# Kernel optimization log

Measured on AMD Instinct MI355X. Metric: run time of the kernel, lower is better.

Reference implementation:

```python
import jax, jax.numpy as jnp
import numpy as np

MARGIN_POS = 1.0
MARGIN_NEG = 0.2
LAMBDA_D = 250.0

B, D, H, W = 2, 128, 64, 64


def setup_inputs() -> dict:
    key = jax.random.key(0)
    k0, k1, k2 = jax.random.split(key, 3)
    descriptors_0 = jax.random.normal(k0, (B, D, H, W), dtype=jnp.float32)
    descriptors_1 = jax.random.normal(k1, (B, D, H, W), dtype=jnp.float32)
    similarity_mask = jax.random.randint(k2, (B, H, W, H, W), 0, 2).astype(jnp.bool_)
    return {
        "descriptors_0": descriptors_0,
        "descriptors_1": descriptors_1,
        "similarity_mask": similarity_mask,
    }


def reference(descriptors_0, descriptors_1, similarity_mask):
    # [B,D,H,W] x [B,D,H,W] -> [B,H,W,H,W] dense pairwise descriptor dot products
    dotprod = jnp.einsum('bdij,bdkl->bijkl', descriptors_0, descriptors_1)
    zero = jnp.zeros((), dtype=dotprod.dtype)
    pos_loss = jnp.maximum(zero, MARGIN_POS - dotprod) * LAMBDA_D
    neg_loss = jnp.maximum(zero, dotprod - MARGIN_NEG)
    return jnp.where(similarity_mask, pos_loss, neg_loss).mean()
```

## Files before the change

kernel.cpp:

```cpp
#include <hip/hip_runtime.h>
#include <hip/hip_bf16.h>
#include <stdint.h>

#define BN 2
#define DN 128
#define MN 4096
#define TOTAL_INV (1.0f / 33554432.0f)

typedef __attribute__((ext_vector_type(8))) short short8;
typedef __attribute__((ext_vector_type(4))) float f32x4;

__device__ static inline unsigned short f2bf(float x) {
  unsigned int u = __float_as_uint(x);
  u += 0x7fffu + ((u >> 16) & 1u);
  return (unsigned short)(u >> 16);
}

__device__ static inline void async16(const void* g, void* l) {
  __builtin_amdgcn_global_load_lds(
      (const __attribute__((address_space(1))) void*)g,
      (__attribute__((address_space(3))) void*)l, 16, 0, 0);
}

__global__ __launch_bounds__(256) void transpose_cvt(
    const float* __restrict__ s0, const float* __restrict__ s1,
    unsigned short* __restrict__ o0, unsigned short* __restrict__ o1) {
  __shared__ float tile[64][65];
  const int tx = threadIdx.x & 63;
  const int ty = threadIdx.x >> 6;
  const int m0 = blockIdx.x * 64;
  const int d0 = blockIdx.y * 64;
  const int b  = blockIdx.z & 1;
  const float* src = (blockIdx.z >> 1) ? s1 : s0;
  unsigned short* dst = (blockIdx.z >> 1) ? o1 : o0;
  src += (size_t)b * DN * MN;
  dst += (size_t)b * MN * DN;
#pragma unroll
  for (int i = 0; i < 16; ++i) {
    int dr = i * 4 + ty;
    tile[dr][tx] = src[(size_t)(d0 + dr) * MN + m0 + tx];
  }
  __syncthreads();
#pragma unroll
  for (int i = 0; i < 16; ++i) {
    int mr = i * 4 + ty;
    dst[(size_t)(m0 + mr) * DN + d0 + tx] = f2bf(tile[tx][mr]);
  }
}

__global__ __launch_bounds__(256) void gemm_loss(
    const unsigned short* __restrict__ A, const unsigned short* __restrict__ Bm,
    const void* __restrict__ maskp, float* __restrict__ out) {
  __shared__ __align__(16) unsigned short As[128 * 32];
  __shared__ __align__(16) unsigned short Bs[128 * 32];
  __shared__ float red[4];
  __shared__ int mask_is_u8;

  const int tid  = threadIdx.x;
  const int lane = tid & 63;
  const int wave = tid >> 6;
  const int wm = wave >> 1, wn = wave & 1;
  const int quad = lane >> 4;
  const int l16  = lane & 15;
  const int bn = blockIdx.x, bm = blockIdx.y, bz = blockIdx.z;

  if (tid == 0) mask_is_u8 = 0;
  __syncthreads();
  if (((const unsigned int*)maskp)[tid] & 0xFFFFFF00u) mask_is_u8 = 1;

  const unsigned short* Ab = A  + (size_t)bz * MN * DN + (size_t)(bm * 128) * DN;
  const unsigned short* Bb = Bm + (size_t)bz * MN * DN + (size_t)(bn * 128) * DN;

  f32x4 acc[4][4];
#pragma unroll
  for (int i = 0; i < 4; ++i)
#pragma unroll
    for (int j = 0; j < 4; ++j) acc[i][j] = (f32x4){0.f, 0.f, 0.f, 0.f};

#pragma unroll
  for (int kt = 0; kt < 4; ++kt) {
    const int k0 = kt * 32;
#pragma unroll
    for (int p = 0; p < 2; ++p) {
      int c = tid + p * 256;
      int row = c >> 2;
      int cq  = c & 3;
      async16(Ab + (size_t)row * DN + k0 + cq * 8, As + c * 8);
      async16(Bb + (size_t)row * DN + k0 + cq * 8, Bs + c * 8);
    }
    __syncthreads();

    short8 af[4], bf[4];
#pragma unroll
    for (int mi = 0; mi < 4; ++mi)
      af[mi] = *(const short8*)(As + (wm * 64 + mi * 16 + l16) * 32 + quad * 8);
#pragma unroll
    for (int ni = 0; ni < 4; ++ni)
      bf[ni] = *(const short8*)(Bs + (wn * 64 + ni * 16 + l16) * 32 + quad * 8);
#pragma unroll
    for (int mi = 0; mi < 4; ++mi)
#pragma unroll
      for (int ni = 0; ni < 4; ++ni)
        acc[mi][ni] = __builtin_amdgcn_mfma_f32_16x16x32_bf16(
            af[mi], bf[ni], acc[mi][ni], 0, 0, 0);
    __syncthreads();
  }

  const size_t mbase =
      ((size_t)bz * MN + (size_t)(bm * 128 + wm * 64)) * MN + (size_t)(bn * 128 + wn * 64);
  const int* mi32 = (const int*)maskp;
  const unsigned char* mu8 = (const unsigned char*)maskp;
  const int u8 = mask_is_u8;
  float lsum = 0.0f;
#pragma unroll
  for (int mi = 0; mi < 4; ++mi) {
#pragma unroll
    for (int ni = 0; ni < 4; ++ni) {
      f32x4 v = acc[mi][ni];
#pragma unroll
      for (int r = 0; r < 4; ++r) {
        int m = mi * 16 + quad * 4 + r;
        int n = ni * 16 + l16;
        size_t idx = mbase + (size_t)m * MN + n;
        int msk = u8 ? (int)mu8[idx] : mi32[idx];
        float dot = v[r];
        float pos = fmaxf(0.0f, 1.0f - dot) * 250.0f;
        float neg = fmaxf(0.0f, dot - 0.2f);
        lsum += msk ? pos : neg;
      }
    }
  }
#pragma unroll
  for (int off = 32; off > 0; off >>= 1) lsum += __shfl_xor(lsum, off);
  if (lane == 0) red[wave] = lsum;
  __syncthreads();
  if (tid == 0) {
    float t = (red[0] + red[1] + red[2] + red[3]) * TOTAL_INV;
    atomicAdd(out, t);
  }
}

extern "C" void kernel_launch(void* const* d_in, const int* in_sizes, int n_in,
                              void* d_out, int out_size, void* d_ws, size_t ws_size,
                              hipStream_t stream) {
  const float* d0 = (const float*)d_in[0];
  const float* d1 = (const float*)d_in[1];
  const void* mask = d_in[2];
  float* out = (float*)d_out;

  unsigned short* Aw = (unsigned short*)d_ws;
  unsigned short* Bw = Aw + (size_t)BN * MN * DN;

  hipMemsetAsync(d_out, 0, sizeof(float), stream);

  dim3 g1(MN / 64, DN / 64, BN * 2), b1(256);
  transpose_cvt<<<g1, b1, 0, stream>>>(d0, d1, Aw, Bw);

  dim3 g2(MN / 128, MN / 128, BN), b2(256);
  gemm_loss<<<g2, b2, 0, stream>>>(Aw, Bw, mask, out);
}
```

Before: 211.1 us.

## Fuse transpose and bf16 conversion into the GEMM-loss kernel

Removes the separate transpose/convert kernel. The GEMM now reads the fp32 [D,M] descriptors directly, converts them to bf16 in registers and writes them transposed into padded LDS (row stride 48) before the MFMA loop. This saves one kernel launch and the round trip through the workspace. In exchange, each of the 2048 blocks reads fp32 data (twice the bytes) with 16 strided scalar loads per thread per k-tile, and the async global-to-LDS copy is replaced by synchronous register staging. The extra global traffic is redundant across the 32 column blocks that share each tile, though most of it should hit in L2.

```diff
diff --git a/kernel.cpp b/kernel.cpp
--- a/kernel.cpp
+++ b/kernel.cpp
@@ -1,58 +1,30 @@
 #include <hip/hip_runtime.h>
-#include <hip/hip_bf16.h>
 #include <stdint.h>
 
 #define BN 2
 #define DN 128
 #define MN 4096
 #define TOTAL_INV (1.0f / 33554432.0f)
+#define LDSTR 48
 
 typedef __attribute__((ext_vector_type(8))) short short8;
 typedef __attribute__((ext_vector_type(4))) float f32x4;
+typedef __attribute__((ext_vector_type(4))) unsigned int u32x4;
 
 __device__ static inline unsigned short f2bf(float x) {
   unsigned int u = __float_as_uint(x);
   u += 0x7fffu + ((u >> 16) & 1u);
   return (unsigned short)(u >> 16);
 }
-
-__device__ static inline void async16(const void* g, void* l) {
-  __builtin_amdgcn_global_load_lds(
-      (const __attribute__((address_space(1))) void*)g,
-      (__attribute__((address_space(3))) void*)l, 16, 0, 0);
+__device__ static inline unsigned int pk2(float a, float b) {
+  return (unsigned int)f2bf(a) | ((unsigned int)f2bf(b) << 16);
 }
 
-__global__ __launch_bounds__(256) void transpose_cvt(
-    const float* __restrict__ s0, const float* __restrict__ s1,
-    unsigned short* __restrict__ o0, unsigned short* __restrict__ o1) {
-  __shared__ float tile[64][65];
-  const int tx = threadIdx.x & 63;
-  const int ty = threadIdx.x >> 6;
-  const int m0 = blockIdx.x * 64;
-  const int d0 = blockIdx.y * 64;
-  const int b  = blockIdx.z & 1;
-  const float* src = (blockIdx.z >> 1) ? s1 : s0;
-  unsigned short* dst = (blockIdx.z >> 1) ? o1 : o0;
-  src += (size_t)b * DN * MN;
-  dst += (size_t)b * MN * DN;
-#pragma unroll
-  for (int i = 0; i < 16; ++i) {
-    int dr = i * 4 + ty;
-    tile[dr][tx] = src[(size_t)(d0 + dr) * MN + m0 + tx];
-  }
-  __syncthreads();
-#pragma unroll
-  for (int i = 0; i < 16; ++i) {
-    int mr = i * 4 + ty;
-    dst[(size_t)(m0 + mr) * DN + d0 + tx] = f2bf(tile[tx][mr]);
-  }
-}
-
-__global__ __launch_bounds__(256) void gemm_loss(
-    const unsigned short* __restrict__ A, const unsigned short* __restrict__ Bm,
+__global__ __launch_bounds__(256) void fused_loss(
+    const float* __restrict__ A, const float* __restrict__ Bg,
     const void* __restrict__ maskp, float* __restrict__ out) {
-  __shared__ __align__(16) unsigned short As[128 * 32];
-  __shared__ __align__(16) unsigned short Bs[128 * 32];
+  __shared__ __align__(16) unsigned short As[128 * LDSTR];
+  __shared__ __align__(16) unsigned short Bs[128 * LDSTR];
   __shared__ float red[4];
   __shared__ int mask_is_u8;
 
@@ -68,8 +40,10 @@
   __syncthreads();
   if (((const unsigned int*)maskp)[tid] & 0xFFFFFF00u) mask_is_u8 = 1;
 
-  const unsigned short* Ab = A  + (size_t)bz * MN * DN + (size_t)(bm * 128) * DN;
-  const unsigned short* Bb = Bm + (size_t)bz * MN * DN + (size_t)(bn * 128) * DN;
+  const int sm = tid & 127;
+  const int dh = (tid >> 7) << 4;
+  const float* Ac = A  + (size_t)bz * DN * MN + (size_t)(bm * 128) + sm;
+  const float* Bc = Bg + (size_t)bz * DN * MN + (size_t)(bn * 128) + sm;
 
   f32x4 acc[4][4];
 #pragma unroll
@@ -77,26 +51,40 @@
 #pragma unroll
     for (int j = 0; j < 4; ++j) acc[i][j] = (f32x4){0.f, 0.f, 0.f, 0.f};
 
+  unsigned short* Ad = As + sm * LDSTR + dh;
+  unsigned short* Bd = Bs + sm * LDSTR + dh;
+  const unsigned short* Ar = As + (wm * 64 + l16) * LDSTR + quad * 8;
+  const unsigned short* Br = Bs + (wn * 64 + l16) * LDSTR + quad * 8;
+
+  for (int kt = 0; kt < 4; ++kt) {
+    const int k0 = kt * 32 + dh;
+    float ra[16], rb[16];
 #pragma unroll
-  for (int kt = 0; kt < 4; ++kt) {
-    const int k0 = kt * 32;
+    for (int j = 0; j < 16; ++j) ra[j] = Ac[(size_t)(k0 + j) * MN];
 #pragma unroll
-    for (int p = 0; p < 2; ++p) {
-      int c = tid + p * 256;
-      int row = c >> 2;
-      int cq  = c & 3;
-      async16(Ab + (size_t)row * DN + k0 + cq * 8, As + c * 8);
-      async16(Bb + (size_t)row * DN + k0 + cq * 8, Bs + c * 8);
-    }
+    for (int j = 0; j < 16; ++j) rb[j] = Bc[(size_t)(k0 + j) * MN];
+    u32x4 w;
+    w = (u32x4){pk2(ra[0], ra[1]),  pk2(ra[2], ra[3]),
+                pk2(ra[4], ra[5]),  pk2(ra[6], ra[7])};
+    *(u32x4*)Ad = w;
+    w = (u32x4){pk2(ra[8], ra[9]),  pk2(ra[10], ra[11]),
+                pk2(ra[12], ra[13]), pk2(ra[14], ra[15])};
+    *(u32x4*)(Ad + 8) = w;
+    w = (u32x4){pk2(rb[0], rb[1]),  pk2(rb[2], rb[3]),
+                pk2(rb[4], rb[5]),  pk2(rb[6], rb[7])};
+    *(u32x4*)Bd = w;
+    w = (u32x4){pk2(rb[8], rb[9]),  pk2(rb[10], rb[11]),
+                pk2(rb[12], rb[13]), pk2(rb[14], rb[15])};
+    *(u32x4*)(Bd + 8) = w;
     __syncthreads();
 
     short8 af[4], bf[4];
 #pragma unroll
     for (int mi = 0; mi < 4; ++mi)
-      af[mi] = *(const short8*)(As + (wm * 64 + mi * 16 + l16) * 32 + quad * 8);
+      af[mi] = *(const short8*)(Ar + mi * 16 * LDSTR);
 #pragma unroll
     for (int ni = 0; ni < 4; ++ni)
-      bf[ni] = *(const short8*)(Bs + (wn * 64 + ni * 16 + l16) * 32 + quad * 8);
+      bf[ni] = *(const short8*)(Br + ni * 16 * LDSTR);
 #pragma unroll
     for (int mi = 0; mi < 4; ++mi)
 #pragma unroll
@@ -146,16 +134,9 @@
   const float* d0 = (const float*)d_in[0];
   const float* d1 = (const float*)d_in[1];
   const void* mask = d_in[2];
-  float* out = (float*)d_out;
-
-  unsigned short* Aw = (unsigned short*)d_ws;
-  unsigned short* Bw = Aw + (size_t)BN * MN * DN;
 
   hipMemsetAsync(d_out, 0, sizeof(float), stream);
 
-  dim3 g1(MN / 64, DN / 64, BN * 2), b1(256);
-  transpose_cvt<<<g1, b1, 0, stream>>>(d0, d1, Aw, Bw);
-
-  dim3 g2(MN / 128, MN / 128, BN), b2(256);
-  gemm_loss<<<g2, b2, 0, stream>>>(Aw, Bw, mask, out);
+  dim3 g(MN / 128, MN / 128, BN), b(256);
+  fused_loss<<<g, b, 0, stream>>>(d0, d1, mask, (float*)d_out);
 }
```

New measurement: 214.0 us. No clear change (+1.4%).

## Double-buffer GEMM K tiles and async-prefetch u8 mask tile into LDS

Applied to the files above, without the earlier changes.

The A/B LDS tiles become double-buffered, so the next K slice loads asynchronously while MFMAs run on the current one, and the per-slice barriers are reduced. For byte masks, the whole 128x128 mask tile is prefetched early into LDS with 16-byte global_load_lds transfers, and the epilogue reads it from LDS instead of making scattered byte loads from global memory. This is meant to hide load latency and coalesce mask traffic. The cost is about 48KB of LDS per block, which may lower occupancy.

```diff
diff --git a/kernel.cpp b/kernel.cpp
--- a/kernel.cpp
+++ b/kernel.cpp
@@ -1,5 +1,4 @@
 #include <hip/hip_runtime.h>
-#include <hip/hip_bf16.h>
 #include <stdint.h>
 
 #define BN 2
@@ -51,8 +50,9 @@
 __global__ __launch_bounds__(256) void gemm_loss(
     const unsigned short* __restrict__ A, const unsigned short* __restrict__ Bm,
     const void* __restrict__ maskp, float* __restrict__ out) {
-  __shared__ __align__(16) unsigned short As[128 * 32];
-  __shared__ __align__(16) unsigned short Bs[128 * 32];
+  __shared__ __align__(16) unsigned short As[2][128 * 32];
+  __shared__ __align__(16) unsigned short Bs[2][128 * 32];
+  __shared__ __align__(16) unsigned char Ms[128 * 128];
   __shared__ float red[4];
   __shared__ int mask_is_u8;
 
@@ -77,40 +77,62 @@
 #pragma unroll
     for (int j = 0; j < 4; ++j) acc[i][j] = (f32x4){0.f, 0.f, 0.f, 0.f};
 
-#pragma unroll
-  for (int kt = 0; kt < 4; ++kt) {
+  auto stage = [&](int sel, int kt) {
     const int k0 = kt * 32;
 #pragma unroll
     for (int p = 0; p < 2; ++p) {
       int c = tid + p * 256;
       int row = c >> 2;
       int cq  = c & 3;
-      async16(Ab + (size_t)row * DN + k0 + cq * 8, As + c * 8);
-      async16(Bb + (size_t)row * DN + k0 + cq * 8, Bs + c * 8);
+      async16(Ab + (size_t)row * DN + k0 + cq * 8, &As[sel][c * 8]);
+      async16(Bb + (size_t)row * DN + k0 + cq * 8, &Bs[sel][c * 8]);
     }
-    __syncthreads();
-
+  };
+  auto compute = [&](int sel) {
     short8 af[4], bf[4];
 #pragma unroll
     for (int mi = 0; mi < 4; ++mi)
-      af[mi] = *(const short8*)(As + (wm * 64 + mi * 16 + l16) * 32 + quad * 8);
+      af[mi] = *(const short8*)(&As[sel][(wm * 64 + mi * 16 + l16) * 32 + quad * 8]);
 #pragma unroll
     for (int ni = 0; ni < 4; ++ni)
-      bf[ni] = *(const short8*)(Bs + (wn * 64 + ni * 16 + l16) * 32 + quad * 8);
+      bf[ni] = *(const short8*)(&Bs[sel][(wn * 64 + ni * 16 + l16) * 32 + quad * 8]);
 #pragma unroll
     for (int mi = 0; mi < 4; ++mi)
 #pragma unroll
       for (int ni = 0; ni < 4; ++ni)
         acc[mi][ni] = __builtin_amdgcn_mfma_f32_16x16x32_bf16(
             af[mi], bf[ni], acc[mi][ni], 0, 0, 0);
-    __syncthreads();
+  };
+
+  stage(0, 0);
+  __syncthreads();
+  const int u8 = mask_is_u8;
+
+  const unsigned char* mg = (const unsigned char*)maskp +
+      ((size_t)bz * MN + (size_t)(bm * 128)) * MN + (size_t)(bn * 128);
+  if (u8) {
+#pragma unroll
+    for (int p = 0; p < 4; ++p) {
+      int c = tid + p * 256;
+      int row = c >> 3, off = (c & 7) * 16;
+      async16(mg + (size_t)row * MN + off, Ms + c * 16);
+    }
   }
+  stage(1, 1);
+  compute(0);
+  __syncthreads();
+  stage(0, 2);
+  compute(1);
+  __syncthreads();
+  stage(1, 3);
+  compute(0);
+  __syncthreads();
+  compute(1);
 
-  const size_t mbase =
+  const size_t gbase =
       ((size_t)bz * MN + (size_t)(bm * 128 + wm * 64)) * MN + (size_t)(bn * 128 + wn * 64);
   const int* mi32 = (const int*)maskp;
-  const unsigned char* mu8 = (const unsigned char*)maskp;
-  const int u8 = mask_is_u8;
+  const int lrow0 = wm * 64, lcol0 = wn * 64;
   float lsum = 0.0f;
 #pragma unroll
   for (int mi = 0; mi < 4; ++mi) {
@@ -121,8 +143,8 @@
       for (int r = 0; r < 4; ++r) {
         int m = mi * 16 + quad * 4 + r;
         int n = ni * 16 + l16;
-        size_t idx = mbase + (size_t)m * MN + n;
-        int msk = u8 ? (int)mu8[idx] : mi32[idx];
+        int msk = u8 ? (int)Ms[(lrow0 + m) * 128 + lcol0 + n]
+                     : mi32[gbase + (size_t)m * MN + n];
         float dot = v[r];
         float pos = fmaxf(0.0f, 1.0f - dot) * 250.0f;
         float neg = fmaxf(0.0f, dot - 0.2f);
```

After: 210.3 us. Within noise of the previous version (-0.4%).

## Use single-wave 64x64 tiles with async mask prefetch and deterministic partial reduction

Applied to the files above, without the earlier changes.

The GEMM-loss kernel now runs one wave per 64x64 output tile instead of four waves per 128x128 tile. Operands are read directly from global memory into MFMA fragments rather than staged through LDS, so block barriers disappear. The u8 mask tile is prefetched into LDS asynchronously, overlapping the matmul, and a grouped block swizzle is meant to improve L2 reuse of operand rows. The per-block atomicAdd and the memset are replaced by a per-tile partials array and a separate single-block reduction kernel, which adds an extra launch and many more small blocks.

```diff
diff --git a/kernel.cpp b/kernel.cpp
--- a/kernel.cpp
+++ b/kernel.cpp
@@ -1,11 +1,13 @@
 #include <hip/hip_runtime.h>
-#include <hip/hip_bf16.h>
 #include <stdint.h>
 
 #define BN 2
 #define DN 128
 #define MN 4096
 #define TOTAL_INV (1.0f / 33554432.0f)
+#define NT 64
+#define NBLK (NT * NT)
+#define PARTIALS (NBLK * BN)
 
 typedef __attribute__((ext_vector_type(8))) short short8;
 typedef __attribute__((ext_vector_type(4))) float f32x4;
@@ -48,28 +50,36 @@
   }
 }
 
-__global__ __launch_bounds__(256) void gemm_loss(
+__global__ __launch_bounds__(64) void gemm_loss(
     const unsigned short* __restrict__ A, const unsigned short* __restrict__ Bm,
-    const void* __restrict__ maskp, float* __restrict__ out) {
-  __shared__ __align__(16) unsigned short As[128 * 32];
-  __shared__ __align__(16) unsigned short Bs[128 * 32];
-  __shared__ float red[4];
-  __shared__ int mask_is_u8;
+    const void* __restrict__ maskp, float* __restrict__ partial) {
+  __shared__ __align__(16) unsigned char Ms[64 * 64];
 
-  const int tid  = threadIdx.x;
-  const int lane = tid & 63;
-  const int wave = tid >> 6;
-  const int wm = wave >> 1, wn = wave & 1;
+  const int lane = threadIdx.x;
   const int quad = lane >> 4;
   const int l16  = lane & 15;
-  const int bn = blockIdx.x, bm = blockIdx.y, bz = blockIdx.z;
+  const int wgid = blockIdx.x;
+  const int bz   = blockIdx.y;
 
-  if (tid == 0) mask_is_u8 = 0;
-  __syncthreads();
-  if (((const unsigned int*)maskp)[tid] & 0xFFFFFF00u) mask_is_u8 = 1;
+  const int swz = (wgid & 7) * (NBLK / 8) + (wgid >> 3);
+  const int bm = swz >> 6;
+  const int bn = swz & 63;
 
-  const unsigned short* Ab = A  + (size_t)bz * MN * DN + (size_t)(bm * 128) * DN;
-  const unsigned short* Bb = Bm + (size_t)bz * MN * DN + (size_t)(bn * 128) * DN;
+  const unsigned int sd = ((const unsigned int*)maskp)[lane];
+  const int u8 = (__ballot((int)(sd & 0xFFFFFF00u)) != 0ull);
+
+  const unsigned char* mg = (const unsigned char*)maskp +
+      ((size_t)bz * MN + (size_t)bm * 64) * MN + (size_t)bn * 64;
+  if (u8) {
+#pragma unroll
+    for (int p = 0; p < 4; ++p) {
+      int c = p * 64 + lane;
+      async16(mg + (size_t)(c >> 2) * MN + (c & 3) * 16, Ms + c * 16);
+    }
+  }
+
+  const unsigned short* Ab = A  + ((size_t)bz * MN + (size_t)bm * 64) * DN;
+  const unsigned short* Bb = Bm + ((size_t)bz * MN + (size_t)bn * 64) * DN;
 
   f32x4 acc[4][4];
 #pragma unroll
@@ -79,38 +89,26 @@
 
 #pragma unroll
   for (int kt = 0; kt < 4; ++kt) {
-    const int k0 = kt * 32;
-#pragma unroll
-    for (int p = 0; p < 2; ++p) {
-      int c = tid + p * 256;
-      int row = c >> 2;
-      int cq  = c & 3;
-      async16(Ab + (size_t)row * DN + k0 + cq * 8, As + c * 8);
-      async16(Bb + (size_t)row * DN + k0 + cq * 8, Bs + c * 8);
-    }
-    __syncthreads();
-
     short8 af[4], bf[4];
 #pragma unroll
     for (int mi = 0; mi < 4; ++mi)
-      af[mi] = *(const short8*)(As + (wm * 64 + mi * 16 + l16) * 32 + quad * 8);
+      af[mi] = *(const short8*)(Ab + (size_t)(mi * 16 + l16) * DN + kt * 32 + quad * 8);
 #pragma unroll
     for (int ni = 0; ni < 4; ++ni)
-      bf[ni] = *(const short8*)(Bs + (wn * 64 + ni * 16 + l16) * 32 + quad * 8);
+      bf[ni] = *(const short8*)(Bb + (size_t)(ni * 16 + l16) * DN + kt * 32 + quad * 8);
 #pragma unroll
     for (int mi = 0; mi < 4; ++mi)
 #pragma unroll
       for (int ni = 0; ni < 4; ++ni)
         acc[mi][ni] = __builtin_amdgcn_mfma_f32_16x16x32_bf16(
             af[mi], bf[ni], acc[mi][ni], 0, 0, 0);
-    __syncthreads();
   }
 
-  const size_t mbase =
-      ((size_t)bz * MN + (size_t)(bm * 128 + wm * 64)) * MN + (size_t)(bn * 128 + wn * 64);
+  asm volatile("s_waitcnt vmcnt(0)" ::: "memory");
+
+  const size_t gbase =
+      ((size_t)bz * MN + (size_t)bm * 64) * MN + (size_t)bn * 64;
   const int* mi32 = (const int*)maskp;
-  const unsigned char* mu8 = (const unsigned char*)maskp;
-  const int u8 = mask_is_u8;
   float lsum = 0.0f;
 #pragma unroll
   for (int mi = 0; mi < 4; ++mi) {
@@ -121,8 +119,8 @@
       for (int r = 0; r < 4; ++r) {
         int m = mi * 16 + quad * 4 + r;
         int n = ni * 16 + l16;
-        size_t idx = mbase + (size_t)m * MN + n;
-        int msk = u8 ? (int)mu8[idx] : mi32[idx];
+        int msk = u8 ? (int)Ms[m * 64 + n]
+                     : mi32[gbase + (size_t)m * MN + n];
         float dot = v[r];
         float pos = fmaxf(0.0f, 1.0f - dot) * 250.0f;
         float neg = fmaxf(0.0f, dot - 0.2f);
@@ -132,12 +130,20 @@
   }
 #pragma unroll
   for (int off = 32; off > 0; off >>= 1) lsum += __shfl_xor(lsum, off);
-  if (lane == 0) red[wave] = lsum;
+  if (lane == 0) partial[(size_t)bz * NBLK + wgid] = lsum;
+}
+
+__global__ __launch_bounds__(256) void reduce_partials(
+    const float* __restrict__ p, float* __restrict__ out) {
+  __shared__ float red[4];
+  const int tid = threadIdx.x;
+  float s = 0.0f;
+  for (int i = tid; i < PARTIALS; i += 256) s += p[i];
+#pragma unroll
+  for (int off = 32; off > 0; off >>= 1) s += __shfl_xor(s, off);
+  if ((tid & 63) == 0) red[tid >> 6] = s;
   __syncthreads();
-  if (tid == 0) {
-    float t = (red[0] + red[1] + red[2] + red[3]) * TOTAL_INV;
-    atomicAdd(out, t);
-  }
+  if (tid == 0) out[0] = (red[0] + red[1] + red[2] + red[3]) * TOTAL_INV;
 }
 
 extern "C" void kernel_launch(void* const* d_in, const int* in_sizes, int n_in,
@@ -150,12 +156,13 @@
 
   unsigned short* Aw = (unsigned short*)d_ws;
   unsigned short* Bw = Aw + (size_t)BN * MN * DN;
-
-  hipMemsetAsync(d_out, 0, sizeof(float), stream);
+  float* partial = (float*)((char*)d_ws + (8u << 20));
 
   dim3 g1(MN / 64, DN / 64, BN * 2), b1(256);
   transpose_cvt<<<g1, b1, 0, stream>>>(d0, d1, Aw, Bw);
 
-  dim3 g2(MN / 128, MN / 128, BN), b2(256);
-  gemm_loss<<<g2, b2, 0, stream>>>(Aw, Bw, mask, out);
+  dim3 g2(NBLK, BN), b2(64);
+  gemm_loss<<<g2, b2, 0, stream>>>(Aw, Bw, mask, partial);
+
+  reduce_partials<<<1, 256, 0, stream>>>(partial, out);
 }
```

New measurement: 236.1 us. 1.12x slower.
